# Kernel optimization log

Hardware: AMD Instinct MI355X
Metric: run time of the kernel (lower is better)

Reference implementation:

```python
import jax, jax.numpy as jnp
import numpy as np

B, L, N = 64, 64, 32           # programs, statement trees per program, nodes per tree
V, E, C, H, OUT = 100000, 128, 128, 100, 104
MAX_DEPTH = 10


def setup_inputs() -> dict:
    key = jax.random.key(0)
    ks = jax.random.split(key, 14)
    rng = np.random.default_rng(0)
    num_trees = B * L
    T = num_trees * N
    # random trees: parent index < node index, depth capped at MAX_DEPTH
    par = np.zeros((num_trees, N), np.int64)
    lev = np.zeros((num_trees, N), np.int64)
    for i in range(1, N):
        p = rng.integers(0, i, size=num_trees)
        pl = lev[np.arange(num_trees), p]
        too_deep = pl + 1 > MAX_DEPTH
        p = np.where(too_deep, 0, p)
        lev[:, i] = np.where(too_deep, 1, pl + 1)
        par[:, i] = p
    base = (np.arange(num_trees) * N)[:, None]
    parent = jnp.asarray((par + base).reshape(-1))          # global parent index
    level = jnp.asarray(lev.reshape(-1))
    tree_id = jnp.asarray(np.repeat(np.arange(num_trees), N))
    node_ids = jax.random.randint(ks[0], (T,), 0, V)
    r = lambda k, shape, s=0.05: (jax.random.normal(k, shape) * s).astype(jnp.float32)
    return {
        'node_ids': node_ids, 'parent': parent, 'level': level, 'tree_id': tree_id,
        'emb': r(ks[1], (V, E), 1.0),
        'W_lin': r(ks[2], (E, C)), 'b_lin': r(ks[3], (C,)),
        'w_ih_f': r(ks[4], (3 * H, C)), 'w_hh_f': r(ks[5], (3 * H, H)),
        'b_ih_f': r(ks[6], (3 * H,)), 'b_hh_f': r(ks[7], (3 * H,)),
        'w_ih_b': r(ks[8], (3 * H, C)), 'w_hh_b': r(ks[9], (3 * H, H)),
        'b_ih_b': r(ks[10], (3 * H,)), 'b_hh_b': r(ks[11], (3 * H,)),
        'fc_w': r(ks[12], (2 * H, OUT)), 'fc_b': r(ks[13], (OUT,)),
    }


def _run_gru(xs, wih, whh, bih, bhh, reverse):
    # xs: [L, B, C]; torch GRU gate math
    def step(hprev, x):
        gi = x @ wih.T + bih
        gh = hprev @ whh.T + bhh
        ir, iz, inn = jnp.split(gi, 3, axis=-1)
        hr, hz, hn = jnp.split(gh, 3, axis=-1)
        rg = jax.nn.sigmoid(ir + hr)
        zg = jax.nn.sigmoid(iz + hz)
        ng = jnp.tanh(inn + rg * hn)
        hnew = (1.0 - zg) * ng + zg * hprev
        return hnew, hnew
    h0 = jnp.zeros((xs.shape[1], whh.shape[1]), xs.dtype)
    _, out = jax.lax.scan(step, h0, xs, reverse=reverse)
    return out  # [L, B, H]


def _forward(node_ids, parent, level, tree_id, emb, W_lin, b_lin,
             w_ih_f, w_hh_f, b_ih_f, b_hh_f, w_ih_b, w_hh_b, b_ih_b, b_hh_b,
             fc_w, fc_b):
    # per-node: h = W*emb(id) + b, then child-sum bottom-up by depth level
    h = emb[node_ids] @ W_lin + b_lin            # [T, C]
    for d in range(MAX_DEPTH, 0, -1):
        contrib = jnp.where((level == d)[:, None], h, 0.0)
        h = h.at[parent].add(contrib)
    # per-tree max pool over all node hidden states -> statement vectors
    stmt = jax.ops.segment_max(h, tree_id, num_segments=B * L)  # [B*L, C]
    xs = stmt.reshape(B, L, C).transpose(1, 0, 2)               # [L, B, C]
    out_f = _run_gru(xs, w_ih_f, w_hh_f, b_ih_f, b_hh_f, reverse=False)
    out_b = _run_gru(xs, w_ih_b, w_hh_b, b_ih_b, b_hh_b, reverse=True)
    gru_out = jnp.concatenate([out_f, out_b], axis=-1)          # [L, B, 2H]
    pooled = gru_out.max(axis=0)                                # [B, 2H]
    return pooled @ fc_w + fc_b                                 # [B, OUT]


def reference(node_ids, parent, level, tree_id, emb, W_lin, b_lin,
              w_ih_f, w_hh_f, b_ih_f, b_hh_f, w_ih_b, w_hh_b, b_ih_b, b_hh_b,
              fc_w, fc_b):
    return _forward(node_ids, parent, level, tree_id, emb, W_lin, b_lin,
                    w_ih_f, w_hh_f, b_ih_f, b_hh_f, w_ih_b, w_hh_b, b_ih_b, b_hh_b,
                    fc_w, fc_b)
```

## Files before the change

### kernel.cpp

```cpp
#include <hip/hip_runtime.h>

typedef _Float16 half8 __attribute__((ext_vector_type(8)));
typedef float f32x4 __attribute__((ext_vector_type(4)));
typedef float f32x16 __attribute__((ext_vector_type(16)));

union H8 { half8 h; float4 f; };

#define EDIM 128
#define CDIM 128
#define HDIM 100
#define ODIM 104

#define OFF_WIH    32768u
#define OFF_WHH    204800u
#define OFF_BIASP  376832u
#define OFF_STMT   379904u
#define OFF_POOL   1428480u

__device__ inline f32x4 zero4() { f32x4 z = {0.f, 0.f, 0.f, 0.f}; return z; }

__device__ inline float fast_exp2(float x) {
  float r; asm("v_exp_f32 %0, %1" : "=v"(r) : "v"(x)); return r;
}
__device__ inline float fast_rcp(float x) {
  float r; asm("v_rcp_f32 %0, %1" : "=v"(r) : "v"(x)); return r;
}
__device__ inline float sigmoid_f(float x) {
  return fast_rcp(1.f + fast_exp2(x * -1.44269504f));
}
__device__ inline float tanh_f(float x) {
  float e = fast_exp2(x * 2.88539008f);
  return fmaf(fast_rcp(1.f + e), -2.f, 1.f);
}

#define HSWZ(row) ((((row) & 3) << 4) ^ (((row) & 12) << 3))

__global__ __launch_bounds__(256, 2) void astnn_tree(
    const int* __restrict__ node_ids, const int* __restrict__ parent,
    const float* __restrict__ emb, const float* __restrict__ W_lin,
    const float* __restrict__ b_lin,
    const float* __restrict__ wihf, const float* __restrict__ whhf,
    const float* __restrict__ bihf, const float* __restrict__ bhhf,
    const float* __restrict__ wihb, const float* __restrict__ whhb,
    const float* __restrict__ bihb, const float* __restrict__ bhhb,
    _Float16* __restrict__ wihfrag, _Float16* __restrict__ whhfrag,
    float* __restrict__ biasP, _Float16* __restrict__ stmt)
{
  __shared__ _Float16 ldsW[16384];
  __shared__ _Float16 ldsA[16384];
  __shared__ int ldsPar[128];
  __shared__ unsigned ldsAnc[128];

  const int t = threadIdx.x, blk = blockIdx.x;
  const int w = t >> 6, l = t & 63;
  const int base = blk * 128;

  if (blk < 87) {
    int gid = blk * 256 + t;
    if (gid < 10752) {
      int i = gid, ll = i & 63, kc = (i >> 6) & 3;
      int rest = i >> 8, nt = rest % 21, d = rest / 21;
      const float* wih = d ? wihb : wihf;
      int n = (nt << 4) + (ll & 15), s = n / 112, j = n - 112 * s;
      int kb = (kc << 5) + ((ll >> 4) << 3);
#pragma unroll
      for (int e = 0; e < 8; e++) {
        int k = kb + e;
        float v = (j < HDIM) ? wih[(s * HDIM + j) * CDIM + k] : 0.f;
        wihfrag[i * 8 + e] = (_Float16)v;
      }
    } else if (gid < 21504) {
      int i = gid - 10752, ll = i & 63, kc = (i >> 6) & 3;
      int rest = i >> 8, nt = rest % 21, d = rest / 21;
      const float* whh = d ? whhb : whhf;
      const float* bhh = d ? bhhb : bhhf;
      int n = (nt << 4) + (ll & 15), s = n / 112, j = n - 112 * s;
      int kb = (kc << 5) + ((ll >> 4) << 3);
#pragma unroll
      for (int e = 0; e < 8; e++) {
        int k = kb + e;
        float v = 0.f;
        if (j < HDIM) {
          if (k < HDIM) v = whh[(s * HDIM + j) * HDIM + k];
          else if (k == HDIM && s == 2) v = bhh[2 * HDIM + j];
        }
        whhfrag[i * 8 + e] = (_Float16)v;
      }
    } else {
      int i = gid - 21504, d = i / 384, col = i % 384, s = col >> 7, j = col & 127;
      const float* bih = d ? bihb : bihf;
      const float* bhh = d ? bhhb : bhhf;
      float v = 0.f;
      if (j < HDIM) { v = bih[s * HDIM + j]; if (s < 2) v += bhh[s * HDIM + j]; }
      biasP[i] = v;
    }
  }

  if (t < 128) ldsPar[t] = parent[base + t] & 31;

  {
#pragma unroll
    for (int i8 = 0; i8 < 8; i8++) {
      int fi = i8 * 256 + t;
      int ll = fi & 63, kc = (fi >> 6) & 3, nt = fi >> 8;
      int n = (nt << 4) + (ll & 15);
      int kb = (kc << 5) + ((ll >> 4) << 3);
#pragma unroll
      for (int e = 0; e < 8; e++)
        ldsW[fi * 8 + e] = (_Float16)W_lin[(kb + e) * CDIM + n];
    }
  }

  {
    const int r = t >> 1, hf = t & 1;
    const int nid = node_ids[base + r];
    const float4* erow = (const float4*)(emb + (size_t)nid * EDIM) + hf * 16;
#pragma unroll
    for (int b2 = 0; b2 < 2; b2++) {
      float4 stage[8];
#pragma unroll
      for (int i = 0; i < 8; i++) stage[i] = erow[b2 * 8 + i];
#pragma unroll
      for (int c4 = 0; c4 < 4; c4++) {
        H8 u;
#pragma unroll
        for (int e = 0; e < 8; e++)
          u.h[e] = (_Float16)(((const float*)&stage[0])[c4 * 8 + e]);
        int c = b2 * 4 + c4;
        int addr = (r * 256 + hf * 128 + c * 16) ^ ((r & 7) << 4);
        *(float4*)((char*)ldsA + addr) = u.f;
      }
    }
  }
  __syncthreads();

  if (t < 128) {
    int tree = t >> 5;
    unsigned mask = 0;
    int cur = t & 31;
#pragma unroll
    for (int it = 0; it < 11; ++it) { mask |= (1u << cur); cur = ldsPar[tree * 32 + cur]; }
    ldsAnc[t] = mask;
  }
  __syncthreads();

  f32x4 acc[2][8];
#pragma unroll
  for (int mt = 0; mt < 2; mt++)
#pragma unroll
    for (int nt = 0; nt < 8; nt++) acc[mt][nt] = zero4();
#pragma unroll
  for (int kc = 0; kc < 4; kc++) {
    half8 af[2];
#pragma unroll
    for (int mt = 0; mt < 2; mt++) {
      int row = (w * 2 + mt) * 16 + (l & 15);
      int addr = (row * 256 + (kc << 6) + ((l >> 4) << 4)) ^ ((row & 7) << 4);
      af[mt] = *(const half8*)((const char*)ldsA + addr);
    }
#pragma unroll
    for (int nt = 0; nt < 8; nt++) {
      half8 bf = *(const half8*)&ldsW[(((nt << 2) | kc) * 64 + l) * 8];
      acc[0][nt] = __builtin_amdgcn_mfma_f32_16x16x32_f16(af[0], bf, acc[0][nt], 0, 0, 0);
      acc[1][nt] = __builtin_amdgcn_mfma_f32_16x16x32_f16(af[1], bf, acc[1][nt], 0, 0, 0);
    }
  }
  __syncthreads();

#pragma unroll
  for (int mt = 0; mt < 2; mt++) {
    const int Mt = w * 2 + mt, tree = Mt >> 1, kc2 = Mt & 1;
#pragma unroll
    for (int nt = 0; nt < 8; nt++) {
      const float bl = b_lin[nt * 16 + (l & 15)];
      const int nt2 = nt >> 1;
      const int ncol = ((nt & 1) << 4) + (l & 15);
#pragma unroll
      for (int reg = 0; reg < 4; reg++) {
        int rowrem = ((l >> 4) << 2) + reg;
        int l2 = ((rowrem >> 3) << 5) + ncol;
        int idx = (((((tree << 2) + nt2) << 1) + kc2) * 64 + l2) * 8 + (rowrem & 7);
        ldsA[idx] = (_Float16)(acc[mt][nt][reg] + bl);
      }
    }
  }
  __syncthreads();

  {
    const int tree = w;
    half8 ancf[2];
#pragma unroll
    for (int kc2 = 0; kc2 < 2; kc2++) {
      H8 u;
#pragma unroll
      for (int e = 0; e < 8; e++) {
        int n = (kc2 << 4) + ((l >> 5) << 3) + e;
        unsigned m = ldsAnc[(tree << 5) + n];
        u.h[e] = (_Float16)(float)((m >> (l & 31)) & 1u);
      }
      ancf[kc2] = u.h;
    }
    f32x16 acc2[4];
#pragma unroll
    for (int nt2 = 0; nt2 < 4; nt2++)
#pragma unroll
      for (int e = 0; e < 16; e++) acc2[nt2][e] = 0.f;
#pragma unroll
    for (int nt2 = 0; nt2 < 4; nt2++)
#pragma unroll
      for (int kc2 = 0; kc2 < 2; kc2++) {
        half8 bf = *(const half8*)&ldsA[(((((tree << 2) + nt2) << 1) + kc2) * 64 + l) * 8];
        acc2[nt2] = __builtin_amdgcn_mfma_f32_32x32x16_f16(ancf[kc2], bf, acc2[nt2], 0, 0, 0);
      }
#pragma unroll
    for (int nt2 = 0; nt2 < 4; nt2++) {
      float m1 = acc2[nt2][0];
#pragma unroll
      for (int e = 1; e < 16; e++) m1 = fmaxf(m1, acc2[nt2][e]);
      m1 = fmaxf(m1, __shfl_xor(m1, 32));
      if (l < 32) {
        int g = blk * 4 + tree;
        int rowp = (g & 63) * 64 + (g >> 6);
        stmt[(size_t)rowp * CDIM + (nt2 << 5) + l] = (_Float16)m1;
      }
    }
  }
}

__global__ __launch_bounds__(448) void astnn_gru(
    const _Float16* __restrict__ whhfrag, const _Float16* __restrict__ wihfrag,
    const _Float16* __restrict__ stmt, const float* __restrict__ biasP,
    float* __restrict__ pooled)
{
  __shared__ _Float16 hlds[4096];
  const int t = threadIdx.x, w = t >> 6, l = t & 63;
  const int mb = blockIdx.x, dir = blockIdx.y;
  for (int i = t; i < 512; i += 448)
    ((float4*)hlds)[i] = make_float4(0.f, 0.f, 0.f, 0.f);
  __syncthreads();
  if (t < 32) {
    int row = t & 15, buf = t >> 4;
    int addr = ((row * 256 + 200) ^ HSWZ(row)) + (buf << 12);
    *(_Float16*)((char*)hlds + addr) = (_Float16)1.0f;
  }

  const int j = (w << 4) + (l & 15);
  const bool jv = (j < HDIM);
  const int rloc = (l >> 4) << 2;
  const int grow = (mb << 4) + rloc;

  int raddr[4], waddr[4];
  {
    int row = l & 15;
#pragma unroll
    for (int kc = 0; kc < 4; kc++)
      raddr[kc] = (row * 256 + (kc << 6) + ((l >> 4) << 4)) ^ HSWZ(row);
#pragma unroll
    for (int reg = 0; reg < 4; reg++) {
      int rw = rloc + reg;
      waddr[reg] = (rw * 256 + (j << 1)) ^ HSWZ(rw);
    }
  }

  half8 bfr[3][4], bfw[3][4];
  {
    const half8* wfh = (const half8*)whhfrag + dir * 5376;
    const half8* wfi = (const half8*)wihfrag + dir * 5376;
#pragma unroll
    for (int s = 0; s < 3; s++)
#pragma unroll
      for (int kc = 0; kc < 4; kc++) {
        int idx = (((s * 7 + w) << 2) + kc) * 64 + l;
        bfr[s][kc] = wfh[idx];
        bfw[s][kc] = wfi[idx];
      }
  }
  const float bias0 = biasP[dir * 384 + j];
  const float bias1 = biasP[dir * 384 + 128 + j];
  const float bias2 = biasP[dir * 384 + 256 + j];

  int soff[4];
#pragma unroll
  for (int kc = 0; kc < 4; kc++)
    soff[kc] = (((mb << 4) + (l & 15)) * 256) + (kc << 6) + ((l >> 4) << 4);
  const ptrdiff_t sstep = dir ? -16384 : 16384;
  const char* sbase = (const char*)stmt + (size_t)(dir ? 63 : 0) * 16384;

  half8 sfA[4], sfB[4];
#pragma unroll
  for (int kc = 0; kc < 4; kc++) sfA[kc] = *(const half8*)(sbase + soff[kc]);
  const char* spre = sbase + sstep;
#pragma unroll
  for (int kc = 0; kc < 4; kc++) sfB[kc] = *(const half8*)(spre + soff[kc]);
  spre += sstep;

  f32x4 giA[3], giB[3];
  giA[0] = f32x4{bias0, bias0, bias0, bias0};
  giA[1] = f32x4{bias1, bias1, bias1, bias1};
  giA[2] = f32x4{bias2, bias2, bias2, bias2};
#pragma unroll
  for (int kc = 0; kc < 4; kc++) {
    giA[0] = __builtin_amdgcn_mfma_f32_16x16x32_f16(sfA[kc], bfw[0][kc], giA[0], 0, 0, 0);
    giA[1] = __builtin_amdgcn_mfma_f32_16x16x32_f16(sfA[kc], bfw[1][kc], giA[1], 0, 0, 0);
    giA[2] = __builtin_amdgcn_mfma_f32_16x16x32_f16(sfA[kc], bfw[2][kc], giA[2], 0, 0, 0);
  }

  float hreg[4], pool[4];
#pragma unroll
  for (int i = 0; i < 4; i++) { hreg[i] = 0.f; pool[i] = -3.0e38f; }
  __syncthreads();

#define GRU_BODY(GIC, GIN, SFsrc, SFdst, ROFF, WOFF, CN, PF)                    \
  {                                                                             \
    half8 afh[4];                                                               \
    _Pragma("unroll")                                                           \
    for (int kc = 0; kc < 4; kc++)                                              \
      afh[kc] = *(const half8*)((const char*)hlds + raddr[kc] + (ROFF));        \
    f32x4 acc0 = GIC[0], acc1 = GIC[1];                                         \
    f32x4 acc2i = GIC[2], acc2h = zero4();                                      \
    _Pragma("unroll")                             \
    for (int kc = 0; kc < 4; kc++) {                                            \
      acc0  = __builtin_amdgcn_mfma_f32_16x16x32_f16(afh[kc], bfr[0][kc], acc0, 0, 0, 0); \
      acc1  = __builtin_amdgcn_mfma_f32_16x16x32_f16(afh[kc], bfr[1][kc], acc1, 0, 0, 0); \
      acc2h = __builtin_amdgcn_mfma_f32_16x16x32_f16(afh[kc], bfr[2][kc], acc2h, 0, 0, 0);\
    }                                                                           \
    if (CN) {     \
      GIN[0] = f32x4{bias0, bias0, bias0, bias0};                               \
      GIN[1] = f32x4{bias1, bias1, bias1, bias1};                               \
      GIN[2] = f32x4{bias2, bias2, bias2, bias2};                               \
      _Pragma("unroll")                                                         \
      for (int kc = 0; kc < 4; kc++) {                                          \
        GIN[0] = __builtin_amdgcn_mfma_f32_16x16x32_f16(SFsrc[kc], bfw[0][kc], GIN[0], 0, 0, 0); \
        GIN[1] = __builtin_amdgcn_mfma_f32_16x16x32_f16(SFsrc[kc], bfw[1][kc], GIN[1], 0, 0, 0); \
        GIN[2] = __builtin_amdgcn_mfma_f32_16x16x32_f16(SFsrc[kc], bfw[2][kc], GIN[2], 0, 0, 0); \
      }                                                                         \
    }                                                                           \
    if (PF) {                                                                   \
      SFdst[0] = *(const half8*)(spre + soff[0]);                               \
      SFdst[1] = *(const half8*)(spre + soff[1]);                               \
      SFdst[2] = *(const half8*)(spre + soff[2]);                               \
      SFdst[3] = *(const half8*)(spre + soff[3]);                               \
      spre += sstep;                                                            \
    }                                                                           \
    _Pragma("unroll")                                                           \
    for (int reg = 0; reg < 4; reg++) {                                         \
      float r = sigmoid_f(acc0[reg]);                                           \
      float z = sigmoid_f(acc1[reg]);                                           \
      float n = tanh_f(fmaf(r, acc2h[reg], acc2i[reg]));                        \
      float hn = n + z * (hreg[reg] - n);                                       \
      hreg[reg] = hn;                                                           \
      pool[reg] = fmaxf(pool[reg], hn);                                         \
      if (jv)                                                                   \
        *(_Float16*)((char*)hlds + waddr[reg] + (WOFF)) = (_Float16)hn;         \
    }                                                                           \
    asm volatile("s_waitcnt lgkmcnt(0)" ::: "memory");                          \
    __builtin_amdgcn_s_barrier();                                               \
    __builtin_amdgcn_sched_barrier(0);                                          \
  }

#pragma unroll 1
  for (int it = 0; it < 31; ++it) {
    GRU_BODY(giA, giB, sfB, sfA, 0, 4096, 1, 1)
    GRU_BODY(giB, giA, sfA, sfB, 4096, 0, 1, 1)
  }
  GRU_BODY(giA, giB, sfB, sfA, 0, 4096, 1, 0)
  GRU_BODY(giB, giA, sfA, sfB, 4096, 0, 0, 0)
#undef GRU_BODY

  if (jv) {
#pragma unroll
    for (int reg = 0; reg < 4; reg++)
      pooled[((size_t)dir << 13) + ((size_t)(grow + reg) << 7) + j] = pool[reg];
  }
}

__global__ __launch_bounds__(128) void astnn_fc(
    const float* __restrict__ pooled, const float* __restrict__ fc_w,
    const float* __restrict__ fc_b, float* __restrict__ out)
{
  __shared__ float p[200];
  const int b = blockIdx.x, t = threadIdx.x;
  for (int i = t; i < 200; i += 128) {
    int d = i / 100, jj = i - d * 100;
    p[i] = pooled[((size_t)d << 13) + (b << 7) + jj];
  }
  __syncthreads();
  if (t < ODIM) {
    float a = fc_b[t];
#pragma unroll 8
    for (int k = 0; k < 200; k++) a = fmaf(p[k], fc_w[k * ODIM + t], a);
    out[b * ODIM + t] = a;
  }
}

extern "C" void kernel_launch(void* const* d_in, const int* in_sizes, int n_in,
                              void* d_out, int out_size, void* d_ws, size_t ws_size,
                              hipStream_t stream)
{
  const int* node_ids = (const int*)d_in[0];
  const int* parent   = (const int*)d_in[1];
  const float* emb    = (const float*)d_in[4];
  const float* W_lin  = (const float*)d_in[5];
  const float* b_lin  = (const float*)d_in[6];
  const float* wihf   = (const float*)d_in[7];
  const float* whhf   = (const float*)d_in[8];
  const float* bihf   = (const float*)d_in[9];
  const float* bhhf   = (const float*)d_in[10];
  const float* wihb   = (const float*)d_in[11];
  const float* whhb   = (const float*)d_in[12];
  const float* bihb   = (const float*)d_in[13];
  const float* bhhb   = (const float*)d_in[14];
  const float* fc_w   = (const float*)d_in[15];
  const float* fc_b   = (const float*)d_in[16];

  char* ws = (char*)d_ws;
  _Float16* wihfrag = (_Float16*)(ws + OFF_WIH);
  _Float16* whhfrag = (_Float16*)(ws + OFF_WHH);
  float* biasP      = (float*)(ws + OFF_BIASP);
  _Float16* stmt    = (_Float16*)(ws + OFF_STMT);
  float* pooled     = (float*)(ws + OFF_POOL);
  float* out        = (float*)d_out;

  astnn_tree<<<1024, 256, 0, stream>>>(node_ids, parent, emb, W_lin, b_lin,
                                       wihf, whhf, bihf, bhhf,
                                       wihb, whhb, bihb, bhhb,
                                       wihfrag, whhfrag, biasP, stmt);
  astnn_gru<<<dim3(4, 2), 448, 0, stream>>>(whhfrag, wihfrag, stmt, biasP, pooled);
  astnn_fc<<<64, 128, 0, stream>>>(pooled, fc_w, fc_b, out);
}
```

Measured before the change: 85.74 us.

## Fuse FC head into GRU kernel with atomics, overlap MFMA with ancestor masks

The final fully connected layer moves into the GRU kernel epilogue. Pooled states are staged in LDS and each direction's partial product is added into the output with atomicAdd after a memset, which removes the separate FC launch and the pooled round trip through global memory. The tree kernel now runs its linear-layer MFMA before the ancestor-mask computation, dropping one barrier, and writes W_lin into LDS as vectorised stores. The GRU accumulates recurrent gates directly into the precomputed gi registers to save register copies. This adds a memset and atomic contention on the output, and the summation order of the two directions is no longer fixed.

```diff
diff --git a/kernel.cpp b/kernel.cpp
--- a/kernel.cpp
+++ b/kernel.cpp
@@ -15,7 +15,6 @@
 #define OFF_WHH    204800u
 #define OFF_BIASP  376832u
 #define OFF_STMT   379904u
-#define OFF_POOL   1428480u
 
 __device__ inline f32x4 zero4() { f32x4 z = {0.f, 0.f, 0.f, 0.f}; return z; }
 
@@ -105,9 +104,11 @@
       int ll = fi & 63, kc = (fi >> 6) & 3, nt = fi >> 8;
       int n = (nt << 4) + (ll & 15);
       int kb = (kc << 5) + ((ll >> 4) << 3);
+      H8 u;
 #pragma unroll
       for (int e = 0; e < 8; e++)
-        ldsW[fi * 8 + e] = (_Float16)W_lin[(kb + e) * CDIM + n];
+        u.h[e] = (_Float16)W_lin[(kb + e) * CDIM + n];
+      *(float4*)&ldsW[fi * 8] = u.f;
     }
   }
 
@@ -134,6 +135,27 @@
   }
   __syncthreads();
 
+  f32x4 acc[2][8];
+#pragma unroll
+  for (int mt = 0; mt < 2; mt++)
+#pragma unroll
+    for (int nt = 0; nt < 8; nt++) acc[mt][nt] = zero4();
+#pragma unroll
+  for (int kc = 0; kc < 4; kc++) {
+    half8 af[2];
+#pragma unroll
+    for (int mt = 0; mt < 2; mt++) {
+      int row = (w * 2 + mt) * 16 + (l & 15);
+      int addr = (row * 256 + (kc << 6) + ((l >> 4) << 4)) ^ ((row & 7) << 4);
+      af[mt] = *(const half8*)((const char*)ldsA + addr);
+    }
+#pragma unroll
+    for (int nt = 0; nt < 8; nt++) {
+      half8 bf = *(const half8*)&ldsW[(((nt << 2) | kc) * 64 + l) * 8];
+      acc[0][nt] = __builtin_amdgcn_mfma_f32_16x16x32_f16(af[0], bf, acc[0][nt], 0, 0, 0);
+      acc[1][nt] = __builtin_amdgcn_mfma_f32_16x16x32_f16(af[1], bf, acc[1][nt], 0, 0, 0);
+    }
+  }
   if (t < 128) {
     int tree = t >> 5;
     unsigned mask = 0;
@@ -141,29 +163,6 @@
 #pragma unroll
     for (int it = 0; it < 11; ++it) { mask |= (1u << cur); cur = ldsPar[tree * 32 + cur]; }
     ldsAnc[t] = mask;
-  }
-  __syncthreads();
-
-  f32x4 acc[2][8];
-#pragma unroll
-  for (int mt = 0; mt < 2; mt++)
-#pragma unroll
-    for (int nt = 0; nt < 8; nt++) acc[mt][nt] = zero4();
-#pragma unroll
-  for (int kc = 0; kc < 4; kc++) {
-    half8 af[2];
-#pragma unroll
-    for (int mt = 0; mt < 2; mt++) {
-      int row = (w * 2 + mt) * 16 + (l & 15);
-      int addr = (row * 256 + (kc << 6) + ((l >> 4) << 4)) ^ ((row & 7) << 4);
-      af[mt] = *(const half8*)((const char*)ldsA + addr);
-    }
-#pragma unroll
-    for (int nt = 0; nt < 8; nt++) {
-      half8 bf = *(const half8*)&ldsW[(((nt << 2) | kc) * 64 + l) * 8];
-      acc[0][nt] = __builtin_amdgcn_mfma_f32_16x16x32_f16(af[0], bf, acc[0][nt], 0, 0, 0);
-      acc[1][nt] = __builtin_amdgcn_mfma_f32_16x16x32_f16(af[1], bf, acc[1][nt], 0, 0, 0);
-    }
   }
   __syncthreads();
 
@@ -230,7 +229,8 @@
 __global__ __launch_bounds__(448) void astnn_gru(
     const _Float16* __restrict__ whhfrag, const _Float16* __restrict__ wihfrag,
     const _Float16* __restrict__ stmt, const float* __restrict__ biasP,
-    float* __restrict__ pooled)
+    const float* __restrict__ fc_w, const float* __restrict__ fc_b,
+    float* __restrict__ out)
 {
   __shared__ _Float16 hlds[4096];
   const int t = threadIdx.x, w = t >> 6, l = t & 63;
@@ -247,7 +247,6 @@
   const int j = (w << 4) + (l & 15);
   const bool jv = (j < HDIM);
   const int rloc = (l >> 4) << 2;
-  const int grow = (mb << 4) + rloc;
 
   int raddr[4], waddr[4];
   {
@@ -316,13 +315,12 @@
     _Pragma("unroll")                                                           \
     for (int kc = 0; kc < 4; kc++)                                              \
       afh[kc] = *(const half8*)((const char*)hlds + raddr[kc] + (ROFF));        \
-    f32x4 acc0 = GIC[0], acc1 = GIC[1];                                         \
-    f32x4 acc2i = GIC[2], acc2h = zero4();                                      \
-    _Pragma("unroll")                             \
+    f32x4 acc2h = zero4();                                                      \
+    _Pragma("unroll")          \
     for (int kc = 0; kc < 4; kc++) {                                            \
-      acc0  = __builtin_amdgcn_mfma_f32_16x16x32_f16(afh[kc], bfr[0][kc], acc0, 0, 0, 0); \
-      acc1  = __builtin_amdgcn_mfma_f32_16x16x32_f16(afh[kc], bfr[1][kc], acc1, 0, 0, 0); \
-      acc2h = __builtin_amdgcn_mfma_f32_16x16x32_f16(afh[kc], bfr[2][kc], acc2h, 0, 0, 0);\
+      GIC[0] = __builtin_amdgcn_mfma_f32_16x16x32_f16(afh[kc], bfr[0][kc], GIC[0], 0, 0, 0); \
+      GIC[1] = __builtin_amdgcn_mfma_f32_16x16x32_f16(afh[kc], bfr[1][kc], GIC[1], 0, 0, 0); \
+      acc2h  = __builtin_amdgcn_mfma_f32_16x16x32_f16(afh[kc], bfr[2][kc], acc2h, 0, 0, 0);  \
     }                                                                           \
     if (CN) {     \
       GIN[0] = f32x4{bias0, bias0, bias0, bias0};                               \
@@ -344,9 +342,9 @@
     }                                                                           \
     _Pragma("unroll")                                                           \
     for (int reg = 0; reg < 4; reg++) {                                         \
-      float r = sigmoid_f(acc0[reg]);                                           \
-      float z = sigmoid_f(acc1[reg]);                                           \
-      float n = tanh_f(fmaf(r, acc2h[reg], acc2i[reg]));                        \
+      float r = sigmoid_f(GIC[0][reg]);                                         \
+      float z = sigmoid_f(GIC[1][reg]);                                         \
+      float n = tanh_f(fmaf(r, acc2h[reg], GIC[2][reg]));                       \
       float hn = n + z * (hreg[reg] - n);                                       \
       hreg[reg] = hn;                                                           \
       pool[reg] = fmaxf(pool[reg], hn);                                         \
@@ -367,29 +365,22 @@
   GRU_BODY(giB, giA, sfA, sfB, 4096, 0, 0, 0)
 #undef GRU_BODY
 
+  float* pl = (float*)hlds;
   if (jv) {
-#pragma unroll
-    for (int reg = 0; reg < 4; reg++)
-      pooled[((size_t)dir << 13) + ((size_t)(grow + reg) << 7) + j] = pool[reg];
-  }
-}
-
-__global__ __launch_bounds__(128) void astnn_fc(
-    const float* __restrict__ pooled, const float* __restrict__ fc_w,
-    const float* __restrict__ fc_b, float* __restrict__ out)
-{
-  __shared__ float p[200];
-  const int b = blockIdx.x, t = threadIdx.x;
-  for (int i = t; i < 200; i += 128) {
-    int d = i / 100, jj = i - d * 100;
-    p[i] = pooled[((size_t)d << 13) + (b << 7) + jj];
-  }
-  __syncthreads();
-  if (t < ODIM) {
-    float a = fc_b[t];
-#pragma unroll 8
-    for (int k = 0; k < 200; k++) a = fmaf(p[k], fc_w[k * ODIM + t], a);
-    out[b * ODIM + t] = a;
+    float4 v = make_float4(pool[0], pool[1], pool[2], pool[3]);
+    *(float4*)(pl + j * 16 + rloc) = v;
+  }
+  __syncthreads();
+  {
+    const float* fcw = fc_w + (size_t)dir * HDIM * ODIM;
+    for (int i = t; i < 16 * ODIM; i += 448) {
+      int row = i / ODIM, o = i - row * ODIM;
+      float s = dir ? 0.f : fc_b[o];
+#pragma unroll 4
+      for (int k = 0; k < HDIM; k++)
+        s = fmaf(pl[k * 16 + row], fcw[k * ODIM + o], s);
+      atomicAdd(&out[(size_t)((mb << 4) + row) * ODIM + o], s);
+    }
   }
 }
 
@@ -418,13 +409,13 @@
   _Float16* whhfrag = (_Float16*)(ws + OFF_WHH);
   float* biasP      = (float*)(ws + OFF_BIASP);
   _Float16* stmt    = (_Float16*)(ws + OFF_STMT);
-  float* pooled     = (float*)(ws + OFF_POOL);
   float* out        = (float*)d_out;
 
+  hipMemsetAsync(d_out, 0, (size_t)out_size * sizeof(float), stream);
   astnn_tree<<<1024, 256, 0, stream>>>(node_ids, parent, emb, W_lin, b_lin,
                                        wihf, whhf, bihf, bhhf,
                                        wihb, whhb, bihb, bhhb,
                                        wihfrag, whhfrag, biasP, stmt);
-  astnn_gru<<<dim3(4, 2), 448, 0, stream>>>(whhfrag, wihfrag, stmt, biasP, pooled);
-  astnn_fc<<<64, 128, 0, stream>>>(pooled, fc_w, fc_b, out);
-}
+  astnn_gru<<<dim3(4, 2), 448, 0, stream>>>(whhfrag, wihfrag, stmt, biasP,
+                                            fc_w, fc_b, out);
+}
```

New measurement: 100.6 us. 17.3% more time.
